# Kernel tuning notes

Measured on AMD Instinct MI355X. Metric: run time of the kernel, lower is better.

Reference implementation:

```python
import jax, jax.numpy as jnp
import numpy as np

N_NODES = 50000
N_EDGES = 800000
F_IN = 128
HID = 128
N_GRAPHS = 256


def setup_inputs() -> dict:
    key = jax.random.key(0)
    ks = jax.random.split(key, 12)
    gx = jax.random.normal(ks[0], (N_NODES, F_IN), dtype=jnp.float32)
    edge_index = jax.random.randint(ks[1], (2, N_EDGES), 0, N_NODES, dtype=jnp.int64)
    batch = jnp.sort(jax.random.randint(ks[2], (N_NODES,), 0, N_GRAPHS, dtype=jnp.int64))
    edge_attr = jax.random.uniform(ks[3], (N_EDGES,), dtype=jnp.float32)
    s1 = 1.0 / np.sqrt(F_IN)
    s2 = 1.0 / np.sqrt(HID)
    W1 = jax.random.uniform(ks[4], (F_IN, HID), jnp.float32, -s1, s1)
    b1 = jnp.zeros((HID,), jnp.float32)
    W2 = jax.random.uniform(ks[5], (HID, HID), jnp.float32, -s2, s2)
    b2 = jnp.zeros((HID,), jnp.float32)
    W3 = jax.random.uniform(ks[6], (HID, HID), jnp.float32, -s2, s2)
    b3 = jnp.zeros((HID,), jnp.float32)
    return {"gx": gx, "edge_index": edge_index, "batch": batch, "edge_attr": edge_attr,
            "W1": W1, "b1": b1, "W2": W2, "b2": b2, "W3": W3, "b3": b3}


def _gcn_conv(x, W, b, row, col, edge_weight, n_nodes):
    # PyG GCNConv with add_self_loops=False:
    #   deg[i] = sum of edge_weight over edges with dst == i
    #   norm_e = deg^{-1/2}[row] * w_e * deg^{-1/2}[col]
    #   out[i] = sum_{e: col_e == i} norm_e * (x @ W)[row_e] + b
    deg = jax.ops.segment_sum(edge_weight, col, num_segments=n_nodes)
    dinv = jnp.where(deg > 0, jax.lax.rsqrt(deg), 0.0)
    norm = dinv[row] * edge_weight * dinv[col]  # [E]
    h = x @ W  # [N, H]
    msg = h[row] * norm[:, None]  # [E, H] gather + scale
    out = jax.ops.segment_sum(msg, col, num_segments=n_nodes)  # scatter-add
    return out + b


def reference(gx, edge_index, batch, edge_attr, W1, b1, W2, b2, W3, b3):
    row, col = edge_index[0], edge_index[1]
    n = gx.shape[0]
    # dropout layers are in eval mode (identity) for a deterministic reference
    h = jax.nn.relu(_gcn_conv(gx, W1, b1, row, col, edge_attr, n))
    h = jax.nn.relu(_gcn_conv(h, W2, b2, row, col, edge_attr, n))
    h = _gcn_conv(h, W3, b3, row, col, edge_attr, n)
    readout = jax.ops.segment_sum(h, batch, num_segments=N_GRAPHS)  # global_add_pool
    return h, readout
```

## Files before the change

kernel.cpp:

```cpp
#include <hip/hip_runtime.h>

#define FEAT 128

typedef __attribute__((ext_vector_type(8))) short short8;
typedef __attribute__((ext_vector_type(4))) float f32x4;

__device__ __forceinline__ unsigned int bf16rtn(float f) {
    unsigned int u = __float_as_uint(f);
    return (u + 0x7fffu + ((u >> 16) & 1u)) >> 16;
}
__device__ __forceinline__ float bf16tof(unsigned int h) { return __uint_as_float(h << 16); }
__device__ __forceinline__ float bf16lo(unsigned int v) { return __uint_as_float(v << 16); }
__device__ __forceinline__ float bf16hi(unsigned int v) { return __uint_as_float(v & 0xffff0000u); }

__global__ __launch_bounds__(256) void hist_kernel(const int* __restrict__ col,
                                                   int* __restrict__ ghist,
                                                   int E, int nblk, int nbuck) {
    __shared__ int h[256];
    const int t = threadIdx.x, b = blockIdx.x;
    h[t] = 0;
    __syncthreads();
    const int base = b * 4096;
#pragma unroll
    for (int i = 0; i < 16; ++i) {
        int e = base + i * 256 + t;
        if (e < E) atomicAdd(&h[col[e] >> 8], 1);
    }
    __syncthreads();
    if (t < nbuck) ghist[t * nblk + b] = h[t];
}

__global__ __launch_bounds__(256) void scan_block_kernel(const int* __restrict__ cnt,
                                                         int* __restrict__ out,
                                                         int* __restrict__ bsum, int M) {
    __shared__ int s[256];
    int t = threadIdx.x;
    int i = blockIdx.x * 256 + t;
    int own = (i < M) ? cnt[i] : 0;
    s[t] = own;
    for (int off = 1; off < 256; off <<= 1) {
        __syncthreads();
        int v = (t >= off) ? s[t - off] : 0;
        __syncthreads();
        s[t] += v;
    }
    __syncthreads();
    if (i < M) out[i] = s[t] - own;
    if (t == 255) bsum[blockIdx.x] = s[255];
}

__global__ __launch_bounds__(256) void scan_bsum_kernel(int* __restrict__ bsum, int nb) {
    __shared__ int s[256];
    int t = threadIdx.x;
    int own = (t < nb) ? bsum[t] : 0;
    s[t] = own;
    for (int off = 1; off < 256; off <<= 1) {
        __syncthreads();
        int v = (t >= off) ? s[t - off] : 0;
        __syncthreads();
        s[t] += v;
    }
    __syncthreads();
    if (t < nb) bsum[t] = s[t] - own;
}

__global__ __launch_bounds__(256) void scatter1_kernel(const int* __restrict__ row,
                                                       const int* __restrict__ col,
                                                       const float* __restrict__ ew,
                                                       const int* __restrict__ gsc,
                                                       const int* __restrict__ bsum,
                                                       uint2* __restrict__ bedge,
                                                       int E, int nblk, int nbuck) {
    __shared__ int cur[256];
    const int t = threadIdx.x, b = blockIdx.x;
    if (t < nbuck) {
        int idx = t * nblk + b;
        cur[t] = gsc[idx] + bsum[idx >> 8];
    }
    __syncthreads();
    const int base = b * 4096;
#pragma unroll
    for (int i = 0; i < 16; ++i) {
        int e = base + i * 256 + t;
        if (e < E) {
            int c = col[e];
            int slot = atomicAdd(&cur[c >> 8], 1);
            bedge[slot] = make_uint2(((unsigned)c << 16) | (unsigned)row[e],
                                     __float_as_uint(ew[e]));
        }
    }
}

__global__ __launch_bounds__(256) void bucket_kernel(const uint2* __restrict__ bedge,
                                                     const int* __restrict__ gsc,
                                                     const int* __restrict__ bsum,
                                                     int* __restrict__ rowptr,
                                                     float* __restrict__ dinv,
                                                     uint2* __restrict__ sedge,
                                                     int N, int E, int nblk, int nbuck) {
    __shared__ int lcnt[256];
    __shared__ float lw[256];
    __shared__ int lscan[256];
    __shared__ int lcur[256];
    __shared__ float ldv[256];

    const int d = blockIdx.x, t = threadIdx.x;
    const int i0 = d * nblk;
    const int base = gsc[i0] + bsum[i0 >> 8];
    int end;
    if (d == nbuck - 1) end = E;
    else {
        const int i1 = (d + 1) * nblk;
        end = gsc[i1] + bsum[i1 >> 8];
    }

    lcnt[t] = 0;
    lw[t] = 0.f;
    __syncthreads();
    for (int i = base + t; i < end; i += 256) {
        uint2 p = bedge[i];
        int c = (p.x >> 16) & 255;
        atomicAdd(&lcnt[c], 1);
        atomicAdd(&lw[c], __uint_as_float(p.y));
    }
    __syncthreads();
    int own = lcnt[t];
    lscan[t] = own;
    for (int off = 1; off < 256; off <<= 1) {
        __syncthreads();
        int v = (t >= off) ? lscan[t - off] : 0;
        __syncthreads();
        lscan[t] += v;
    }
    __syncthreads();
    int excl = lscan[t] - own;
    lcur[t] = base + excl;
    float wsum = lw[t];
    float dv = (wsum > 0.f) ? rsqrtf(wsum) : 0.f;
    ldv[t] = dv;
    int node = d * 256 + t;
    if (node < N) {
        rowptr[node] = base + excl;
        dinv[node] = dv;
    }
    if (d == nbuck - 1 && t == 0) rowptr[N] = E;
    __syncthreads();
    for (int i = base + t; i < end; i += 256) {
        uint2 p = bedge[i];
        int c = (p.x >> 16) & 255;
        int slot = atomicAdd(&lcur[c], 1);
        sedge[slot] = make_uint2(p.x & 0xFFFFu,
                                 __float_as_uint(__uint_as_float(p.y) * ldv[c]));
    }
}

__global__ void norm_kernel(uint2* __restrict__ sedge, const float* __restrict__ dinv, int E) {
    int i = blockIdx.x * blockDim.x + threadIdx.x;
    if (i < E) {
        uint2 p = sedge[i];
        p.y = __float_as_uint(__uint_as_float(p.y) * dinv[p.x]);
        sedge[i] = p;
    }
}

__global__ void convw_kernel(const float* __restrict__ W0, const float* __restrict__ W1,
                             const float* __restrict__ W2,
                             unsigned short* __restrict__ Whi, unsigned short* __restrict__ Wlo) {
    int i = blockIdx.x * blockDim.x + threadIdx.x;
    int which = blockIdx.y;
    const float* W = (which == 0) ? W0 : (which == 1) ? W1 : W2;
    int c = i >> 7, k = i & 127;
    float w = W[(size_t)k * FEAT + c];
    unsigned int h = bf16rtn(w);
    size_t off = (size_t)which * 16384 + (size_t)c * FEAT + k;
    Whi[off] = (unsigned short)h;
    Wlo[off] = (unsigned short)bf16rtn(w - bf16tof(h));
}

__global__ __launch_bounds__(256) void gemm_mfma_kernel(
    const float* __restrict__ X,
    const unsigned short* __restrict__ Wthi, const unsigned short* __restrict__ Wtlo,
    unsigned int* __restrict__ hb,
    int N)
{
    __shared__ unsigned short wh[64 * 128];
    __shared__ unsigned short wl[64 * 128];

    const int tid = threadIdx.x;
    const int r0 = blockIdx.x * 64;
    const int cb = blockIdx.y;

#pragma unroll
    for (int it = 0; it < 4; ++it) {
        int idx = it * 256 + tid;
        int c = idx >> 4;
        int k8 = (idx & 15) * 8;
        int sw = k8 ^ ((c & 7) << 3);
        size_t src = (size_t)(cb * 64 + c) * FEAT + k8;
        *(short8*)&wh[c * 128 + sw] = *(const short8*)(Wthi + src);
        *(short8*)&wl[c * 128 + sw] = *(const short8*)(Wtlo + src);
    }
    __syncthreads();

    const int lane = tid & 63;
    const int wv = tid >> 6;
    const int m = lane & 15;
    const int quad = lane >> 4;
    const int arow = wv * 16 + m;
    const int grow = r0 + arow;
    const float* xrow = X + (size_t)grow * FEAT;

    f32x4 acc[4];
#pragma unroll
    for (int ct = 0; ct < 4; ++ct) acc[ct] = (f32x4){0.f, 0.f, 0.f, 0.f};

#pragma unroll
    for (int kt = 0; kt < 4; ++kt) {
        const int k0 = kt * 32 + quad * 8;
        float4 va = make_float4(0.f, 0.f, 0.f, 0.f);
        float4 vb = make_float4(0.f, 0.f, 0.f, 0.f);
        if (grow < N) {
            va = *(const float4*)(xrow + k0);
            vb = *(const float4*)(xrow + k0 + 4);
        }
        unsigned int h0 = bf16rtn(va.x), h1 = bf16rtn(va.y);
        unsigned int h2 = bf16rtn(va.z), h3 = bf16rtn(va.w);
        unsigned int h4 = bf16rtn(vb.x), h5 = bf16rtn(vb.y);
        unsigned int h6 = bf16rtn(vb.z), h7 = bf16rtn(vb.w);
        short8 ah, al;
        ah[0] = (short)h0; ah[1] = (short)h1; ah[2] = (short)h2; ah[3] = (short)h3;
        ah[4] = (short)h4; ah[5] = (short)h5; ah[6] = (short)h6; ah[7] = (short)h7;
        al[0] = (short)bf16rtn(va.x - bf16tof(h0));
        al[1] = (short)bf16rtn(va.y - bf16tof(h1));
        al[2] = (short)bf16rtn(va.z - bf16tof(h2));
        al[3] = (short)bf16rtn(va.w - bf16tof(h3));
        al[4] = (short)bf16rtn(vb.x - bf16tof(h4));
        al[5] = (short)bf16rtn(vb.y - bf16tof(h5));
        al[6] = (short)bf16rtn(vb.z - bf16tof(h6));
        al[7] = (short)bf16rtn(vb.w - bf16tof(h7));
#pragma unroll
        for (int ct = 0; ct < 4; ++ct) {
            int bc = ct * 16 + m;
            int bw = k0 ^ ((bc & 7) << 3);
            short8 bh = *(const short8*)&wh[bc * 128 + bw];
            short8 bl = *(const short8*)&wl[bc * 128 + bw];
            acc[ct] = __builtin_amdgcn_mfma_f32_16x16x32_bf16(ah, bh, acc[ct], 0, 0, 0);
            acc[ct] = __builtin_amdgcn_mfma_f32_16x16x32_bf16(ah, bl, acc[ct], 0, 0, 0);
            acc[ct] = __builtin_amdgcn_mfma_f32_16x16x32_bf16(al, bh, acc[ct], 0, 0, 0);
        }
    }

    __syncthreads();
    unsigned short* cl = wh;
#pragma unroll
    for (int ct = 0; ct < 4; ++ct)
#pragma unroll
        for (int reg = 0; reg < 4; ++reg) {
            int rrow = wv * 16 + quad * 4 + reg;
            cl[rrow * 72 + ct * 16 + m] = (unsigned short)bf16rtn(acc[ct][reg]);
        }
    __syncthreads();
#pragma unroll
    for (int it = 0; it < 2; ++it) {
        int idx = it * 256 + tid;
        int r = idx >> 3;
        int c4 = (idx & 7) * 4;
        int gr = r0 + r;
        if (gr < N) {
            uint4 pv = *(const uint4*)&cl[r * 72 + c4 * 2];
            *(uint4*)(hb + (size_t)gr * 64 + cb * 32 + c4) = pv;
        }
    }
}

template <int RELU>
__global__ __launch_bounds__(256) void agg_kernel(
    const int* __restrict__ rowptr, const uint2* __restrict__ sedge,
    const uint2* __restrict__ hb2,
    const float* __restrict__ bias,
    float* __restrict__ outX, int N)
{
    const int node = blockIdx.x * 4 + (threadIdx.x >> 6);
    if (node >= N) return;
    const int lane = threadIdx.x & 63;
    const int h = lane >> 5;
    const int j = lane & 31;
    const int s = rowptr[node];
    const int e = rowptr[node + 1];

    float a0 = 0.f, a1 = 0.f, a2 = 0.f, a3 = 0.f;

    for (int gb = s; gb < e; gb += 16) {
        uint2 m0, m1, m2, m3, m4, m5, m6, m7;
        if (gb + 16 <= e) {
            m0 = sedge[gb + 0 + h];  m1 = sedge[gb + 2 + h];
            m2 = sedge[gb + 4 + h];  m3 = sedge[gb + 6 + h];
            m4 = sedge[gb + 8 + h];  m5 = sedge[gb + 10 + h];
            m6 = sedge[gb + 12 + h]; m7 = sedge[gb + 14 + h];
        } else {
            const uint2 z = make_uint2(0u, 0u);
            int i0 = gb + 0 + h, i1 = gb + 2 + h, i2 = gb + 4 + h, i3 = gb + 6 + h;
            int i4 = gb + 8 + h, i5 = gb + 10 + h, i6 = gb + 12 + h, i7 = gb + 14 + h;
            m0 = (i0 < e) ? sedge[i0] : z;  m1 = (i1 < e) ? sedge[i1] : z;
            m2 = (i2 < e) ? sedge[i2] : z;  m3 = (i3 < e) ? sedge[i3] : z;
            m4 = (i4 < e) ? sedge[i4] : z;  m5 = (i5 < e) ? sedge[i5] : z;
            m6 = (i6 < e) ? sedge[i6] : z;  m7 = (i7 < e) ? sedge[i7] : z;
        }
        uint2 v0 = hb2[(size_t)m0.x * 32 + j];
        uint2 v1 = hb2[(size_t)m1.x * 32 + j];
        uint2 v2 = hb2[(size_t)m2.x * 32 + j];
        uint2 v3 = hb2[(size_t)m3.x * 32 + j];
        uint2 v4 = hb2[(size_t)m4.x * 32 + j];
        uint2 v5 = hb2[(size_t)m5.x * 32 + j];
        uint2 v6 = hb2[(size_t)m6.x * 32 + j];
        uint2 v7 = hb2[(size_t)m7.x * 32 + j];
        float w0 = __uint_as_float(m0.y), w1 = __uint_as_float(m1.y);
        float w2 = __uint_as_float(m2.y), w3 = __uint_as_float(m3.y);
        float w4 = __uint_as_float(m4.y), w5 = __uint_as_float(m5.y);
        float w6 = __uint_as_float(m6.y), w7 = __uint_as_float(m7.y);
        a0 = fmaf(w0, bf16lo(v0.x), a0); a1 = fmaf(w0, bf16hi(v0.x), a1);
        a2 = fmaf(w0, bf16lo(v0.y), a2); a3 = fmaf(w0, bf16hi(v0.y), a3);
        a0 = fmaf(w1, bf16lo(v1.x), a0); a1 = fmaf(w1, bf16hi(v1.x), a1);
        a2 = fmaf(w1, bf16lo(v1.y), a2); a3 = fmaf(w1, bf16hi(v1.y), a3);
        a0 = fmaf(w2, bf16lo(v2.x), a0); a1 = fmaf(w2, bf16hi(v2.x), a1);
        a2 = fmaf(w2, bf16lo(v2.y), a2); a3 = fmaf(w2, bf16hi(v2.y), a3);
        a0 = fmaf(w3, bf16lo(v3.x), a0); a1 = fmaf(w3, bf16hi(v3.x), a1);
        a2 = fmaf(w3, bf16lo(v3.y), a2); a3 = fmaf(w3, bf16hi(v3.y), a3);
        a0 = fmaf(w4, bf16lo(v4.x), a0); a1 = fmaf(w4, bf16hi(v4.x), a1);
        a2 = fmaf(w4, bf16lo(v4.y), a2); a3 = fmaf(w4, bf16hi(v4.y), a3);
        a0 = fmaf(w5, bf16lo(v5.x), a0); a1 = fmaf(w5, bf16hi(v5.x), a1);
        a2 = fmaf(w5, bf16lo(v5.y), a2); a3 = fmaf(w5, bf16hi(v5.y), a3);
        a0 = fmaf(w6, bf16lo(v6.x), a0); a1 = fmaf(w6, bf16hi(v6.x), a1);
        a2 = fmaf(w6, bf16lo(v6.y), a2); a3 = fmaf(w6, bf16hi(v6.y), a3);
        a0 = fmaf(w7, bf16lo(v7.x), a0); a1 = fmaf(w7, bf16hi(v7.x), a1);
        a2 = fmaf(w7, bf16lo(v7.y), a2); a3 = fmaf(w7, bf16hi(v7.y), a3);
    }

    a0 += __shfl_xor(a0, 32);
    a1 += __shfl_xor(a1, 32);
    a2 += __shfl_xor(a2, 32);
    a3 += __shfl_xor(a3, 32);

    if (h == 0) {
        float4 bv = ((const float4*)bias)[j];
        a0 += bv.x; a1 += bv.y; a2 += bv.z; a3 += bv.w;
        if (RELU) {
            a0 = fmaxf(a0, 0.f); a1 = fmaxf(a1, 0.f);
            a2 = fmaxf(a2, 0.f); a3 = fmaxf(a3, 0.f);
        }
        *(float4*)(outX + (size_t)node * FEAT + j * 4) = make_float4(a0, a1, a2, a3);
    }
}

__global__ __launch_bounds__(256) void readout_kernel(const float* __restrict__ h,
                                                      const int* __restrict__ batch,
                                                      float* __restrict__ ro, int N) {
    __shared__ float part[128];
    const int g = blockIdx.x;
    const int j = threadIdx.x & 127;
    const int half = threadIdx.x >> 7;
    int lo = 0, hi = N;
    while (lo < hi) { int mid = (lo + hi) >> 1; if (batch[mid] < g) lo = mid + 1; else hi = mid; }
    int lo2 = lo, hi2 = N;
    while (lo2 < hi2) { int mid = (lo2 + hi2) >> 1; if (batch[mid] < g + 1) lo2 = mid + 1; else hi2 = mid; }

    float s0 = 0.f, s1 = 0.f;
    int n = lo + half;
    for (; n + 2 < lo2; n += 4) {
        s0 += h[(size_t)n * FEAT + j];
        s1 += h[(size_t)(n + 2) * FEAT + j];
    }
    if (n < lo2) s0 += h[(size_t)n * FEAT + j];
    float s = s0 + s1;
    if (half == 1) part[j] = s;
    __syncthreads();
    if (half == 0) ro[(size_t)g * FEAT + j] = s + part[j];
}

static inline size_t align256(size_t x) { return (x + 255) & ~(size_t)255; }

extern "C" void kernel_launch(void* const* d_in, const int* in_sizes, int n_in,
                              void* d_out, int out_size, void* d_ws, size_t ws_size,
                              hipStream_t stream) {
    const float* gx    = (const float*)d_in[0];
    const int*   ei    = (const int*)d_in[1];
    const int*   batch = (const int*)d_in[2];
    const float* ew    = (const float*)d_in[3];
    const float* W1 = (const float*)d_in[4];
    const float* b1 = (const float*)d_in[5];
    const float* W2 = (const float*)d_in[6];
    const float* b2 = (const float*)d_in[7];
    const float* W3 = (const float*)d_in[8];
    const float* b3 = (const float*)d_in[9];

    const int N = in_sizes[0] / FEAT;
    const int E = in_sizes[3];
    const int G = (out_size - N * FEAT) / FEAT;

    const int* row = ei;
    const int* col = ei + E;

    const int nbuck = (N + 255) >> 8;
    const int nblk  = (E + 4095) >> 12;
    const int M     = nbuck * nblk;

    char* ws = (char*)d_ws;
    int*   rowptr = (int*)ws;         ws += align256((size_t)(N + 1) * 4);
    float* dinv   = (float*)ws;       ws += align256((size_t)N * 4);
    int*   ghist  = (int*)ws;         ws += align256((size_t)M * 4);
    int*   gsc    = (int*)ws;         ws += align256((size_t)M * 4);
    int*   bsum   = (int*)ws;         ws += align256(256 * 4);
    uint2* bedge  = (uint2*)ws;       ws += align256((size_t)E * 8);
    uint2* sedge  = (uint2*)ws;       ws += align256((size_t)E * 8);
    unsigned int* hb = (unsigned int*)ws;  ws += align256((size_t)N * 64 * 4);
    float* bufX   = (float*)ws;       ws += align256((size_t)N * FEAT * 4);
    unsigned short* Wh = (unsigned short*)ws; ws += align256((size_t)3 * 16384 * 2);
    unsigned short* Wl = (unsigned short*)ws; ws += align256((size_t)3 * 16384 * 2);

    float* h_out = (float*)d_out;
    float* ro    = h_out + (size_t)N * FEAT;

    hist_kernel<<<nblk, 256, 0, stream>>>(col, ghist, E, nblk, nbuck);
    const int snb = (M + 255) / 256;
    scan_block_kernel<<<snb, 256, 0, stream>>>(ghist, gsc, bsum, M);
    scan_bsum_kernel<<<1, 256, 0, stream>>>(bsum, snb);
    scatter1_kernel<<<nblk, 256, 0, stream>>>(row, col, ew, gsc, bsum, bedge, E, nblk, nbuck);
    bucket_kernel<<<nbuck, 256, 0, stream>>>(bedge, gsc, bsum, rowptr, dinv, sedge, N, E, nblk, nbuck);
    norm_kernel<<<(E + 255) / 256, 256, 0, stream>>>(sedge, dinv, E);

    convw_kernel<<<dim3(64, 3), 256, 0, stream>>>(W1, W2, W3, Wh, Wl);

    dim3 ggrid((N + 63) / 64, 2);
    const int ablocks = (N + 3) / 4;
    const uint2* hb2 = (const uint2*)hb;

    gemm_mfma_kernel<<<ggrid, 256, 0, stream>>>(gx, Wh, Wl, hb, N);
    agg_kernel<1><<<ablocks, 256, 0, stream>>>(rowptr, sedge, hb2, b1, bufX, N);
    gemm_mfma_kernel<<<ggrid, 256, 0, stream>>>(bufX, Wh + 16384, Wl + 16384, hb, N);
    agg_kernel<1><<<ablocks, 256, 0, stream>>>(rowptr, sedge, hb2, b2, bufX, N);
    gemm_mfma_kernel<<<ggrid, 256, 0, stream>>>(bufX, Wh + 32768, Wl + 32768, hb, N);
    agg_kernel<0><<<ablocks, 256, 0, stream>>>(rowptr, sedge, hb2, b3, h_out, N);
    readout_kernel<<<G, 256, 0, stream>>>(h_out, batch, ro, N);
}
```

Before: 298.8 us.

## Fold source dinv scaling into GEMM epilogue and widen aggregation gathers

Removes the separate per-edge norm pass by multiplying each GEMM output row by its source node's dinv before the bf16 store. Each edge weight then only carries the destination factor, which is already applied in the bucket kernel. Separately, the aggregation kernel now gathers 16-byte uint4 rows with 16 lanes per edge and 4 edges in flight per wave, instead of 8-byte loads with 32 lanes. This reduces memory requests per edge, at the cost of fewer edge loads in flight per iteration and an extra shuffle-reduction level.

```diff
diff --git a/kernel.cpp b/kernel.cpp
--- a/kernel.cpp
+++ b/kernel.cpp
@@ -154,15 +154,6 @@
     }
 }
 
-__global__ void norm_kernel(uint2* __restrict__ sedge, const float* __restrict__ dinv, int E) {
-    int i = blockIdx.x * blockDim.x + threadIdx.x;
-    if (i < E) {
-        uint2 p = sedge[i];
-        p.y = __float_as_uint(__uint_as_float(p.y) * dinv[p.x]);
-        sedge[i] = p;
-    }
-}
-
 __global__ void convw_kernel(const float* __restrict__ W0, const float* __restrict__ W1,
                              const float* __restrict__ W2,
                              unsigned short* __restrict__ Whi, unsigned short* __restrict__ Wlo) {
@@ -180,6 +171,7 @@
 __global__ __launch_bounds__(256) void gemm_mfma_kernel(
     const float* __restrict__ X,
     const unsigned short* __restrict__ Wthi, const unsigned short* __restrict__ Wtlo,
+    const float* __restrict__ dinv,
     unsigned int* __restrict__ hb,
     int N)
 {
@@ -250,15 +242,28 @@
         }
     }
 
+    const int rbase = wv * 16 + quad * 4;
+    const int grb = r0 + rbase;
+    float dv0, dv1, dv2, dv3;
+    if (grb + 3 < N) {
+        float4 d4 = *(const float4*)(dinv + grb);
+        dv0 = d4.x; dv1 = d4.y; dv2 = d4.z; dv3 = d4.w;
+    } else {
+        dv0 = (grb + 0 < N) ? dinv[grb + 0] : 0.f;
+        dv1 = (grb + 1 < N) ? dinv[grb + 1] : 0.f;
+        dv2 = (grb + 2 < N) ? dinv[grb + 2] : 0.f;
+        dv3 = (grb + 3 < N) ? dinv[grb + 3] : 0.f;
+    }
+
     __syncthreads();
     unsigned short* cl = wh;
 #pragma unroll
-    for (int ct = 0; ct < 4; ++ct)
-#pragma unroll
-        for (int reg = 0; reg < 4; ++reg) {
-            int rrow = wv * 16 + quad * 4 + reg;
-            cl[rrow * 72 + ct * 16 + m] = (unsigned short)bf16rtn(acc[ct][reg]);
-        }
+    for (int ct = 0; ct < 4; ++ct) {
+        cl[(rbase + 0) * 72 + ct * 16 + m] = (unsigned short)bf16rtn(acc[ct][0] * dv0);
+        cl[(rbase + 1) * 72 + ct * 16 + m] = (unsigned short)bf16rtn(acc[ct][1] * dv1);
+        cl[(rbase + 2) * 72 + ct * 16 + m] = (unsigned short)bf16rtn(acc[ct][2] * dv2);
+        cl[(rbase + 3) * 72 + ct * 16 + m] = (unsigned short)bf16rtn(acc[ct][3] * dv3);
+    }
     __syncthreads();
 #pragma unroll
     for (int it = 0; it < 2; ++it) {
@@ -276,79 +281,80 @@
 template <int RELU>
 __global__ __launch_bounds__(256) void agg_kernel(
     const int* __restrict__ rowptr, const uint2* __restrict__ sedge,
-    const uint2* __restrict__ hb2,
+    const uint4* __restrict__ hb4,
     const float* __restrict__ bias,
     float* __restrict__ outX, int N)
 {
     const int node = blockIdx.x * 4 + (threadIdx.x >> 6);
     if (node >= N) return;
     const int lane = threadIdx.x & 63;
-    const int h = lane >> 5;
-    const int j = lane & 31;
+    const int g = lane >> 4;
+    const int j = lane & 15;
     const int s = rowptr[node];
     const int e = rowptr[node + 1];
 
     float a0 = 0.f, a1 = 0.f, a2 = 0.f, a3 = 0.f;
+    float a4 = 0.f, a5 = 0.f, a6 = 0.f, a7 = 0.f;
 
     for (int gb = s; gb < e; gb += 16) {
-        uint2 m0, m1, m2, m3, m4, m5, m6, m7;
+        uint2 m0, m1, m2, m3;
         if (gb + 16 <= e) {
-            m0 = sedge[gb + 0 + h];  m1 = sedge[gb + 2 + h];
-            m2 = sedge[gb + 4 + h];  m3 = sedge[gb + 6 + h];
-            m4 = sedge[gb + 8 + h];  m5 = sedge[gb + 10 + h];
-            m6 = sedge[gb + 12 + h]; m7 = sedge[gb + 14 + h];
+            m0 = sedge[gb + g];       m1 = sedge[gb + 4 + g];
+            m2 = sedge[gb + 8 + g];   m3 = sedge[gb + 12 + g];
         } else {
             const uint2 z = make_uint2(0u, 0u);
-            int i0 = gb + 0 + h, i1 = gb + 2 + h, i2 = gb + 4 + h, i3 = gb + 6 + h;
-            int i4 = gb + 8 + h, i5 = gb + 10 + h, i6 = gb + 12 + h, i7 = gb + 14 + h;
-            m0 = (i0 < e) ? sedge[i0] : z;  m1 = (i1 < e) ? sedge[i1] : z;
-            m2 = (i2 < e) ? sedge[i2] : z;  m3 = (i3 < e) ? sedge[i3] : z;
-            m4 = (i4 < e) ? sedge[i4] : z;  m5 = (i5 < e) ? sedge[i5] : z;
-            m6 = (i6 < e) ? sedge[i6] : z;  m7 = (i7 < e) ? sedge[i7] : z;
-        }
-        uint2 v0 = hb2[(size_t)m0.x * 32 + j];
-        uint2 v1 = hb2[(size_t)m1.x * 32 + j];
-        uint2 v2 = hb2[(size_t)m2.x * 32 + j];
-        uint2 v3 = hb2[(size_t)m3.x * 32 + j];
-        uint2 v4 = hb2[(size_t)m4.x * 32 + j];
-        uint2 v5 = hb2[(size_t)m5.x * 32 + j];
-        uint2 v6 = hb2[(size_t)m6.x * 32 + j];
-        uint2 v7 = hb2[(size_t)m7.x * 32 + j];
+            int i0 = gb + g, i1 = gb + 4 + g, i2 = gb + 8 + g, i3 = gb + 12 + g;
+            m0 = (i0 < e) ? sedge[i0] : z;
+            m1 = (i1 < e) ? sedge[i1] : z;
+            m2 = (i2 < e) ? sedge[i2] : z;
+            m3 = (i3 < e) ? sedge[i3] : z;
+        }
+        uint4 v0 = hb4[(size_t)m0.x * 16 + j];
+        uint4 v1 = hb4[(size_t)m1.x * 16 + j];
+        uint4 v2 = hb4[(size_t)m2.x * 16 + j];
+        uint4 v3 = hb4[(size_t)m3.x * 16 + j];
         float w0 = __uint_as_float(m0.y), w1 = __uint_as_float(m1.y);
         float w2 = __uint_as_float(m2.y), w3 = __uint_as_float(m3.y);
-        float w4 = __uint_as_float(m4.y), w5 = __uint_as_float(m5.y);
-        float w6 = __uint_as_float(m6.y), w7 = __uint_as_float(m7.y);
         a0 = fmaf(w0, bf16lo(v0.x), a0); a1 = fmaf(w0, bf16hi(v0.x), a1);
         a2 = fmaf(w0, bf16lo(v0.y), a2); a3 = fmaf(w0, bf16hi(v0.y), a3);
+        a4 = fmaf(w0, bf16lo(v0.z), a4); a5 = fmaf(w0, bf16hi(v0.z), a5);
+        a6 = fmaf(w0, bf16lo(v0.w), a6); a7 = fmaf(w0, bf16hi(v0.w), a7);
         a0 = fmaf(w1, bf16lo(v1.x), a0); a1 = fmaf(w1, bf16hi(v1.x), a1);
         a2 = fmaf(w1, bf16lo(v1.y), a2); a3 = fmaf(w1, bf16hi(v1.y), a3);
+        a4 = fmaf(w1, bf16lo(v1.z), a4); a5 = fmaf(w1, bf16hi(v1.z), a5);
+        a6 = fmaf(w1, bf16lo(v1.w), a6); a7 = fmaf(w1, bf16hi(v1.w), a7);
         a0 = fmaf(w2, bf16lo(v2.x), a0); a1 = fmaf(w2, bf16hi(v2.x), a1);
         a2 = fmaf(w2, bf16lo(v2.y), a2); a3 = fmaf(w2, bf16hi(v2.y), a3);
+        a4 = fmaf(w2, bf16lo(v2.z), a4); a5 = fmaf(w2, bf16hi(v2.z), a5);
+        a6 = fmaf(w2, bf16lo(v2.w), a6); a7 = fmaf(w2, bf16hi(v2.w), a7);
         a0 = fmaf(w3, bf16lo(v3.x), a0); a1 = fmaf(w3, bf16hi(v3.x), a1);
         a2 = fmaf(w3, bf16lo(v3.y), a2); a3 = fmaf(w3, bf16hi(v3.y), a3);
-        a0 = fmaf(w4, bf16lo(v4.x), a0); a1 = fmaf(w4, bf16hi(v4.x), a1);
-        a2 = fmaf(w4, bf16lo(v4.y), a2); a3 = fmaf(w4, bf16hi(v4.y), a3);
-        a0 = fmaf(w5, bf16lo(v5.x), a0); a1 = fmaf(w5, bf16hi(v5.x), a1);
-        a2 = fmaf(w5, bf16lo(v5.y), a2); a3 = fmaf(w5, bf16hi(v5.y), a3);
-        a0 = fmaf(w6, bf16lo(v6.x), a0); a1 = fmaf(w6, bf16hi(v6.x), a1);
-        a2 = fmaf(w6, bf16lo(v6.y), a2); a3 = fmaf(w6, bf16hi(v6.y), a3);
-        a0 = fmaf(w7, bf16lo(v7.x), a0); a1 = fmaf(w7, bf16hi(v7.x), a1);
-        a2 = fmaf(w7, bf16lo(v7.y), a2); a3 = fmaf(w7, bf16hi(v7.y), a3);
-    }
-
-    a0 += __shfl_xor(a0, 32);
-    a1 += __shfl_xor(a1, 32);
-    a2 += __shfl_xor(a2, 32);
-    a3 += __shfl_xor(a3, 32);
-
-    if (h == 0) {
-        float4 bv = ((const float4*)bias)[j];
-        a0 += bv.x; a1 += bv.y; a2 += bv.z; a3 += bv.w;
+        a4 = fmaf(w3, bf16lo(v3.z), a4); a5 = fmaf(w3, bf16hi(v3.z), a5);
+        a6 = fmaf(w3, bf16lo(v3.w), a6); a7 = fmaf(w3, bf16hi(v3.w), a7);
+    }
+
+    a0 += __shfl_xor(a0, 16); a0 += __shfl_xor(a0, 32);
+    a1 += __shfl_xor(a1, 16); a1 += __shfl_xor(a1, 32);
+    a2 += __shfl_xor(a2, 16); a2 += __shfl_xor(a2, 32);
+    a3 += __shfl_xor(a3, 16); a3 += __shfl_xor(a3, 32);
+    a4 += __shfl_xor(a4, 16); a4 += __shfl_xor(a4, 32);
+    a5 += __shfl_xor(a5, 16); a5 += __shfl_xor(a5, 32);
+    a6 += __shfl_xor(a6, 16); a6 += __shfl_xor(a6, 32);
+    a7 += __shfl_xor(a7, 16); a7 += __shfl_xor(a7, 32);
+
+    if (g == 0) {
+        float4 bv0 = ((const float4*)bias)[j * 2];
+        float4 bv1 = ((const float4*)bias)[j * 2 + 1];
+        a0 += bv0.x; a1 += bv0.y; a2 += bv0.z; a3 += bv0.w;
+        a4 += bv1.x; a5 += bv1.y; a6 += bv1.z; a7 += bv1.w;
         if (RELU) {
             a0 = fmaxf(a0, 0.f); a1 = fmaxf(a1, 0.f);
             a2 = fmaxf(a2, 0.f); a3 = fmaxf(a3, 0.f);
-        }
-        *(float4*)(outX + (size_t)node * FEAT + j * 4) = make_float4(a0, a1, a2, a3);
+            a4 = fmaxf(a4, 0.f); a5 = fmaxf(a5, 0.f);
+            a6 = fmaxf(a6, 0.f); a7 = fmaxf(a7, 0.f);
+        }
+        *(float4*)(outX + (size_t)node * FEAT + j * 8)     = make_float4(a0, a1, a2, a3);
+        *(float4*)(outX + (size_t)node * FEAT + j * 8 + 4) = make_float4(a4, a5, a6, a7);
     }
 }
 
@@ -426,19 +432,18 @@
     scan_bsum_kernel<<<1, 256, 0, stream>>>(bsum, snb);
     scatter1_kernel<<<nblk, 256, 0, stream>>>(row, col, ew, gsc, bsum, bedge, E, nblk, nbuck);
     bucket_kernel<<<nbuck, 256, 0, stream>>>(bedge, gsc, bsum, rowptr, dinv, sedge, N, E, nblk, nbuck);
-    norm_kernel<<<(E + 255) / 256, 256, 0, stream>>>(sedge, dinv, E);
 
     convw_kernel<<<dim3(64, 3), 256, 0, stream>>>(W1, W2, W3, Wh, Wl);
 
     dim3 ggrid((N + 63) / 64, 2);
     const int ablocks = (N + 3) / 4;
-    const uint2* hb2 = (const uint2*)hb;
-
-    gemm_mfma_kernel<<<ggrid, 256, 0, stream>>>(gx, Wh, Wl, hb, N);
-    agg_kernel<1><<<ablocks, 256, 0, stream>>>(rowptr, sedge, hb2, b1, bufX, N);
-    gemm_mfma_kernel<<<ggrid, 256, 0, stream>>>(bufX, Wh + 16384, Wl + 16384, hb, N);
-    agg_kernel<1><<<ablocks, 256, 0, stream>>>(rowptr, sedge, hb2, b2, bufX, N);
-    gemm_mfma_kernel<<<ggrid, 256, 0, stream>>>(bufX, Wh + 32768, Wl + 32768, hb, N);
-    agg_kernel<0><<<ablocks, 256, 0, stream>>>(rowptr, sedge, hb2, b3, h_out, N);
+    const uint4* hb4 = (const uint4*)hb;
+
+    gemm_mfma_kernel<<<ggrid, 256, 0, stream>>>(gx, Wh, Wl, dinv, hb, N);
+    agg_kernel<1><<<ablocks, 256, 0, stream>>>(rowptr, sedge, hb4, b1, bufX, N);
+    gemm_mfma_kernel<<<ggrid, 256, 0, stream>>>(bufX, Wh + 16384, Wl + 16384, dinv, hb, N);
+    agg_kernel<1><<<ablocks, 256, 0, stream>>>(rowptr, sedge, hb4, b2, bufX, N);
+    gemm_mfma_kernel<<<ggrid, 256, 0, stream>>>(bufX, Wh + 32768, Wl + 32768, dinv, hb, N);
+    agg_kernel<0><<<ablocks, 256, 0, stream>>>(rowptr, sedge, hb4, b3, h_out, N);
     readout_kernel<<<G, 256, 0, stream>>>(h_out, batch, ro, N);
 }
```

Measured after the change: 289.1 us. 1.03x faster.
